# Kernel tuning notes

Measured on AMD Instinct MI355X. Metric: run time of the kernel, lower is better.

Reference implementation:

```python
import jax, jax.numpy as jnp
import numpy as np

N_NODES = 50000
N_EDGES = 800000
IN_DIM = 128
ADD = 8
HIDDEN = 256
OUT_DIM = 128


def gcn_conv(x, src, dst, W, b, n_nodes):
    """PyG GCNConv: linear -> sym-normalized scatter-add with self-loops -> bias."""
    loop = jnp.arange(n_nodes, dtype=src.dtype)
    s = jnp.concatenate([src, loop])
    d = jnp.concatenate([dst, loop])
    deg = jax.ops.segment_sum(jnp.ones(s.shape[0], dtype=x.dtype), d, num_segments=n_nodes)
    dinv = jnp.where(deg > 0, jax.lax.rsqrt(deg), 0.0)
    norm = dinv[s] * dinv[d]                       # [E+N]
    h = x @ W                                      # [N, F_out]
    msg = h[s] * norm[:, None]                     # [E+N, F_out]
    out = jax.ops.segment_sum(msg, d, num_segments=n_nodes)
    return out + b


def prelu(x, a):
    return jnp.where(x >= 0, x, a * x)


def setup_inputs() -> dict:
    key = jax.random.key(0)
    ks = jax.random.split(key, 8)
    x = jax.random.normal(ks[0], (N_NODES, IN_DIM), dtype=jnp.float32)
    edge_index = jax.random.randint(ks[1], (2, N_EDGES), 0, N_NODES, dtype=jnp.int64)
    id_vec = jax.random.normal(ks[2], (ADD,), dtype=jnp.float32)
    # Glorot-ish init for linear weights, PReLU slope 0.25 (torch default)
    W1 = jax.random.normal(ks[3], (IN_DIM + ADD, HIDDEN), dtype=jnp.float32) * 0.05
    b1 = jnp.zeros((HIDDEN,), dtype=jnp.float32)
    a1 = jnp.full((HIDDEN,), 0.25, dtype=jnp.float32)
    W2 = jax.random.normal(ks[4], (HIDDEN, OUT_DIM), dtype=jnp.float32) * 0.05
    b2 = jnp.zeros((OUT_DIM,), dtype=jnp.float32)
    a2 = jnp.full((OUT_DIM,), 0.25, dtype=jnp.float32)
    return {"x": x, "edge_index": edge_index, "id": id_vec,
            "W1": W1, "b1": b1, "a1": a1, "W2": W2, "b2": b2, "a2": a2}


def reference(x, edge_index, id, W1, b1, a1, W2, b2, a2):
    n = x.shape[0]
    src, dst = edge_index[0], edge_index[1]
    # tile id vector onto every node and concat along features
    xi = jnp.concatenate([x, jnp.broadcast_to(id[None, :], (n, id.shape[0]))], axis=1)
    h = gcn_conv(xi, src, dst, W1, b1, n)
    h = prelu(h, a1)
    h = gcn_conv(h, src, dst, W2, b2, n)
    h = prelu(h, a2)
    return h
```

## Files before the change

### kernel.cpp

```cpp
#include <hip/hip_runtime.h>


constexpr int NN = 50000;
constexpr int NE = 800000;
constexpr int NBUCK = 196;
constexpr int TILE = 2048;
constexpr int NSCAT = (NE + TILE - 1) / TILE;
constexpr int NAGG = NN / 4;

typedef __attribute__((ext_vector_type(8))) short short8;
typedef __attribute__((ext_vector_type(4))) float floatx4;

__device__ inline void bsplit(float v, unsigned short& hi, unsigned short& lo) {
  unsigned u = __float_as_uint(v);
  hi = (unsigned short)(u >> 16);
  float rem = v - __uint_as_float(u & 0xffff0000u);
  lo = (unsigned short)(__float_as_uint(rem) >> 16);
}

__device__ inline unsigned short bf16_rtne(float v) {
  unsigned u = __float_as_uint(v);
  return (unsigned short)((u + 0x7fffu + ((u >> 16) & 1u)) >> 16);
}

__device__ inline float bflo(unsigned u) { return __uint_as_float(u << 16); }
__device__ inline float bfhi(unsigned u) { return __uint_as_float(u & 0xffff0000u); }

template <int K, int N>
__device__ inline void pack_one(const float* __restrict__ W, unsigned short* __restrict__ Bhi,
                                unsigned short* __restrict__ Blo, int id) {
  constexpr int KC = K / 32;
  int j = id & 7;
  int lane = (id >> 3) & 63;
  int rest = id >> 9;
  int c = rest % KC;
  int nt = rest / KC;
  int k = c * 32 + (lane >> 4) * 8 + j;
  int n = nt * 16 + (lane & 15);
  unsigned short hi, lo;
  bsplit(W[(size_t)k * N + n], hi, lo);
  Bhi[id] = hi;
  Blo[id] = lo;
}

__global__ __launch_bounds__(256) void front_kernel(
    const int* __restrict__ ei, int* __restrict__ tilecnt,
    const float* __restrict__ W1, const float* __restrict__ W2,
    const float* __restrict__ idv,
    unsigned short* __restrict__ B1hi, unsigned short* __restrict__ B1lo,
    unsigned short* __restrict__ B2hi, unsigned short* __restrict__ B2lo,
    float* __restrict__ cvec) {
  int t = threadIdx.x;
  if (blockIdx.x < NSCAT) {
    __shared__ int h[NBUCK];
    for (int i = t; i < NBUCK; i += 256) h[i] = 0;
    __syncthreads();
    int base = blockIdx.x * TILE;
    int end = base + TILE; if (end > NE) end = NE;
    for (int e = base + t; e < end; e += 256) atomicAdd(&h[ei[NE + e] >> 8], 1);
    __syncthreads();
    for (int i = t; i < NBUCK; i += 256) tilecnt[blockIdx.x * NBUCK + i] = h[i];
  } else {
    int id = (blockIdx.x - NSCAT) * 256 + t;
    if (id < 32768) {
      pack_one<128, 256>(W1, B1hi, B1lo, id);
    } else if (id < 65536) {
      pack_one<256, 128>(W2, B2hi, B2lo, id - 32768);
    } else if (id < 65536 + 256) {
      int m = id - 65536;
      float c = 0.f;
#pragma unroll
      for (int j = 0; j < 8; ++j) c += idv[j] * W1[(128 + j) * 256 + m];
      cvec[m] = c;
    }
  }
}

__global__ __launch_bounds__(256) void tile_scan_a_kernel(const int* __restrict__ tilecnt,
                                                          int* __restrict__ tpre,
                                                          int* __restrict__ bcnt) {
  __shared__ int sm[256];
  int b = blockIdx.x, t = threadIdx.x;
  int i0 = 2 * t, i1 = 2 * t + 1;
  int v0 = (i0 < NSCAT) ? tilecnt[i0 * NBUCK + b] : 0;
  int v1 = (i1 < NSCAT) ? tilecnt[i1 * NBUCK + b] : 0;
  int s = v0 + v1;
  sm[t] = s;
  __syncthreads();
  for (int off = 1; off < 256; off <<= 1) {
    int u = (t >= off) ? sm[t - off] : 0;
    __syncthreads();
    sm[t] += u;
    __syncthreads();
  }
  int ex = sm[t] - s;
  if (i0 < NSCAT) tpre[i0 * NBUCK + b] = ex;
  if (i1 < NSCAT) tpre[i1 * NBUCK + b] = ex + v0;
  if (t == 255) bcnt[b] = sm[255];
}

__global__ __launch_bounds__(256) void bucket_scatter_kernel(
    const int* __restrict__ ei, const int* __restrict__ tilecnt,
    const int* __restrict__ tpre, const int* __restrict__ bcnt,
    unsigned* __restrict__ ebuf) {
  __shared__ int lbase[NBUCK], gb[NBUCK], lcur[NBUCK], ssc[256], bscan[256];
  __shared__ unsigned stage[TILE];
  int t = threadIdx.x;
  int tile = blockIdx.x;
  int base = tile * TILE;
  int cntTile = NE - base; if (cntTile > TILE) cntTile = TILE;
  int bv = (t < NBUCK) ? bcnt[t] : 0;
  bscan[t] = bv;
  int h = (t < NBUCK) ? tilecnt[tile * NBUCK + t] : 0;
  ssc[t] = h;
  __syncthreads();
  for (int off = 1; off < 256; off <<= 1) {
    int u1 = (t >= off) ? ssc[t - off] : 0;
    int u2 = (t >= off) ? bscan[t - off] : 0;
    __syncthreads();
    ssc[t] += u1;
    bscan[t] += u2;
    __syncthreads();
  }
  if (t < NBUCK) {
    int ex = ssc[t] - h;
    lbase[t] = ex;
    lcur[t] = ex;
    gb[t] = (bscan[t] - bv) + tpre[tile * NBUCK + t];
  }
  __syncthreads();
  for (int e = base + t; e < base + cntTile; e += 256) {
    int s = ei[e];
    int d = ei[NE + e];
    int b = d >> 8;
    int pos = atomicAdd(&lcur[b], 1);
    stage[pos] = ((unsigned)(d & 255) << 16) | (unsigned)s;
  }
  __syncthreads();
  for (int i = t; i < cntTile; i += 256) {
    int lo = 0, hi = NBUCK - 1;
    while (lo < hi) {
      int mid = (lo + hi + 1) >> 1;
      if (lbase[mid] <= i) lo = mid; else hi = mid - 1;
    }
    ebuf[gb[lo] + (i - lbase[lo])] = stage[i];
  }
}

__global__ __launch_bounds__(256) void bucket_csr_kernel(
    const unsigned* __restrict__ ebuf, const int* __restrict__ bcnt,
    const float* __restrict__ x,
    int* __restrict__ offs, int* __restrict__ col,
    float* __restrict__ dinv, unsigned short* __restrict__ xsb) {
  __shared__ int cnt[256], cur[256], sums[256], bscan[256];
  __shared__ float dinvs[256];
  __shared__ int g0s;
  int b = blockIdx.x, t = threadIdx.x;
  int node0 = b << 8;
  cnt[t] = 0;
  int bv = (t < NBUCK) ? bcnt[t] : 0;
  bscan[t] = bv;
  __syncthreads();
  for (int off = 1; off < 256; off <<= 1) {
    int u = (t >= off) ? bscan[t - off] : 0;
    __syncthreads();
    bscan[t] += u;
    __syncthreads();
  }
  if (t == b) g0s = bscan[t] - bv;
  __syncthreads();
  int g0 = g0s, g1 = g0 + bcnt[b];
  for (int i = g0 + t; i < g1; i += 256) atomicAdd(&cnt[ebuf[i] >> 16], 1);
  __syncthreads();
  int c = cnt[t];
  sums[t] = c;
  __syncthreads();
  for (int off = 1; off < 256; off <<= 1) {
    int u = (t >= off) ? sums[t - off] : 0;
    __syncthreads();
    sums[t] += u;
    __syncthreads();
  }
  int ex = sums[t] - c;
  cur[t] = ex;
  float dval = rsqrtf((float)(c + 1));
  dinvs[t] = dval;
  int node = node0 + t;
  if (node < NN) {
    offs[node] = g0 + ex;
    dinv[node] = dval;
  }
  __syncthreads();
  for (int i = g0 + t; i < g1; i += 256) {
    unsigned v = ebuf[i];
    int pos = atomicAdd(&cur[v >> 16], 1);
    col[g0 + pos] = (int)(v & 0xffffu);
  }
  for (int i = t; i < 256 * 32; i += 256) {
    int ln = i >> 5;
    int n2 = node0 + ln;
    if (n2 >= NN) continue;
    float dd = dinvs[ln];
    float4 v = ((const float4*)x)[(size_t)n2 * 32 + (i & 31)];
    ushort4 o;
    o.x = bf16_rtne(v.x * dd);
    o.y = bf16_rtne(v.y * dd);
    o.z = bf16_rtne(v.z * dd);
    o.w = bf16_rtne(v.w * dd);
    ((ushort4*)xsb)[(size_t)n2 * 32 + (i & 31)] = o;
  }
  if (b == 0 && t == 0) offs[NN] = NE;
}

template <int MODE>
__global__ __launch_bounds__(256) void agg_kernel(
    const unsigned short* __restrict__ in, const float* __restrict__ dinv,
    const int* __restrict__ offs, const int* __restrict__ col,
    const float* __restrict__ bias, const float* __restrict__ alpha,
    unsigned short* __restrict__ outhi, unsigned short* __restrict__ outlo,
    float* __restrict__ outf, float* __restrict__ Svec) {
  int t = threadIdx.x;
  if (MODE == 0 && blockIdx.x >= NAGG) {
    int d = (blockIdx.x - NAGG) * 256 + t;
    if (d < NN) {
      float s = 0.f;
      int end = offs[d + 1];
      for (int p = offs[d]; p < end; ++p) s += dinv[col[p]];
      float dd = dinv[d];
      Svec[d] = dd * (dd + s);
    }
    return;
  }
  const uint2* inb = (const uint2*)in;
  int node = blockIdx.x * 4 + (t >> 6);
  int lane = t & 63;
  int r = lane & 31;
  int half = lane >> 5;
  int beg = offs[node], end = offs[node + 1];

  float4 a0 = make_float4(0.f, 0.f, 0.f, 0.f);
  float4 a1 = make_float4(0.f, 0.f, 0.f, 0.f);
  float4 a2 = make_float4(0.f, 0.f, 0.f, 0.f);
  float4 a3 = make_float4(0.f, 0.f, 0.f, 0.f);
  int p = beg + half;
  for (; p + 14 < end; p += 16) {
    int s0 = col[p];      int s1 = col[p + 2];
    int s2 = col[p + 4];  int s3 = col[p + 6];
    int s4 = col[p + 8];  int s5 = col[p + 10];
    int s6 = col[p + 12]; int s7 = col[p + 14];
    uint2 v0 = inb[(size_t)s0 * 32 + r];
    uint2 v1 = inb[(size_t)s1 * 32 + r];
    uint2 v2 = inb[(size_t)s2 * 32 + r];
    uint2 v3 = inb[(size_t)s3 * 32 + r];
    uint2 v4 = inb[(size_t)s4 * 32 + r];
    uint2 v5 = inb[(size_t)s5 * 32 + r];
    uint2 v6 = inb[(size_t)s6 * 32 + r];
    uint2 v7 = inb[(size_t)s7 * 32 + r];
    a0.x += bflo(v0.x); a0.y += bfhi(v0.x); a0.z += bflo(v0.y); a0.w += bfhi(v0.y);
    a1.x += bflo(v1.x); a1.y += bfhi(v1.x); a1.z += bflo(v1.y); a1.w += bfhi(v1.y);
    a2.x += bflo(v2.x); a2.y += bfhi(v2.x); a2.z += bflo(v2.y); a2.w += bfhi(v2.y);
    a3.x += bflo(v3.x); a3.y += bfhi(v3.x); a3.z += bflo(v3.y); a3.w += bfhi(v3.y);
    a0.x += bflo(v4.x); a0.y += bfhi(v4.x); a0.z += bflo(v4.y); a0.w += bfhi(v4.y);
    a1.x += bflo(v5.x); a1.y += bfhi(v5.x); a1.z += bflo(v5.y); a1.w += bfhi(v5.y);
    a2.x += bflo(v6.x); a2.y += bfhi(v6.x); a2.z += bflo(v6.y); a2.w += bfhi(v6.y);
    a3.x += bflo(v7.x); a3.y += bfhi(v7.x); a3.z += bflo(v7.y); a3.w += bfhi(v7.y);
  }
  for (; p + 2 < end; p += 4) {
    int s0 = col[p];
    int s1 = col[p + 2];
    uint2 v0 = inb[(size_t)s0 * 32 + r];
    uint2 v1 = inb[(size_t)s1 * 32 + r];
    a0.x += bflo(v0.x); a0.y += bfhi(v0.x); a0.z += bflo(v0.y); a0.w += bfhi(v0.y);
    a1.x += bflo(v1.x); a1.y += bfhi(v1.x); a1.z += bflo(v1.y); a1.w += bfhi(v1.y);
  }
  if (p < end) {
    uint2 v0 = inb[(size_t)col[p] * 32 + r];
    a0.x += bflo(v0.x); a0.y += bfhi(v0.x); a0.z += bflo(v0.y); a0.w += bfhi(v0.y);
  }
  float4 acc = make_float4((a0.x + a1.x) + (a2.x + a3.x), (a0.y + a1.y) + (a2.y + a3.y),
                           (a0.z + a1.z) + (a2.z + a3.z), (a0.w + a1.w) + (a2.w + a3.w));
  acc.x += __shfl_xor(acc.x, 32);
  acc.y += __shfl_xor(acc.y, 32);
  acc.z += __shfl_xor(acc.z, 32);
  acc.w += __shfl_xor(acc.w, 32);

  float dd = dinv[node];
  if (half == 0) {
    uint2 sv = inb[(size_t)node * 32 + r];
    acc.x = dd * (acc.x + bflo(sv.x));
    acc.y = dd * (acc.y + bfhi(sv.x));
    acc.z = dd * (acc.z + bflo(sv.y));
    acc.w = dd * (acc.w + bfhi(sv.y));
    if (MODE == 0) {
      ushort4 h4, l4;
      bsplit(acc.x, h4.x, l4.x);
      bsplit(acc.y, h4.y, l4.y);
      bsplit(acc.z, h4.z, l4.z);
      bsplit(acc.w, h4.w, l4.w);
      ((ushort4*)outhi)[(size_t)node * 32 + r] = h4;
      ((ushort4*)outlo)[(size_t)node * 32 + r] = l4;
    } else {
      float4 b = ((const float4*)bias)[r];
      float4 al = ((const float4*)alpha)[r];
      acc.x += b.x; acc.y += b.y; acc.z += b.z; acc.w += b.w;
      acc.x = (acc.x >= 0.f) ? acc.x : al.x * acc.x;
      acc.y = (acc.y >= 0.f) ? acc.y : al.y * acc.y;
      acc.z = (acc.z >= 0.f) ? acc.z : al.z * acc.z;
      acc.w = (acc.w >= 0.f) ? acc.w : al.w * acc.w;
      ((float4*)outf)[(size_t)node * 32 + r] = acc;
    }
  }
}

template <int K, int N, int MODE, int ASPLIT>
__global__ __launch_bounds__(256) void gemm_mfma_kernel(
    const unsigned short* __restrict__ Ahi, const unsigned short* __restrict__ Alo,
    const unsigned short* __restrict__ Bhi, const unsigned short* __restrict__ Blo,
    const float* __restrict__ Svec, const float* __restrict__ cvec,
    const float* __restrict__ bias, const float* __restrict__ alpha,
    const float* __restrict__ rowscale, unsigned short* __restrict__ Cb) {
  constexpr int KC = K / 32;
  constexpr int NT = N / 16;
  int wave = threadIdx.x >> 6;
  int lane = threadIdx.x & 63;
  int row0 = blockIdx.x * 64 + wave * 16;
  if (row0 >= NN) return;
  int m = lane & 15, quad = lane >> 4;
  int arow = row0 + m;

  short8 ah[KC], al[KC];
  const unsigned short* ap = Ahi + (size_t)arow * K + quad * 8;
#pragma unroll
  for (int c = 0; c < KC; ++c) ah[c] = *(const short8*)(ap + c * 32);
  if (ASPLIT) {
    const unsigned short* alp = Alo + (size_t)arow * K + quad * 8;
#pragma unroll
    for (int c = 0; c < KC; ++c) al[c] = *(const short8*)(alp + c * 32);
  }

  float sv[4];
#pragma unroll
  for (int i = 0; i < 4; ++i) {
    int r = row0 + quad * 4 + i;
    sv[i] = (MODE == 1) ? Svec[r] : rowscale[r];
  }

#pragma unroll 1
  for (int nt = 0; nt < NT; ++nt) {
    floatx4 acc = {0.f, 0.f, 0.f, 0.f};
#pragma unroll
    for (int c = 0; c < KC; ++c) {
      short8 bh = *(const short8*)(Bhi + ((size_t)(nt * KC + c) * 64 + lane) * 8);
      short8 bl = *(const short8*)(Blo + ((size_t)(nt * KC + c) * 64 + lane) * 8);
      acc = __builtin_amdgcn_mfma_f32_16x16x32_bf16(ah[c], bh, acc, 0, 0, 0);
      acc = __builtin_amdgcn_mfma_f32_16x16x32_bf16(ah[c], bl, acc, 0, 0, 0);
      if (ASPLIT) acc = __builtin_amdgcn_mfma_f32_16x16x32_bf16(al[c], bh, acc, 0, 0, 0);
    }
    int c0 = nt * 16 + m;
    if (MODE == 1) {
      float cv = cvec[c0], bb = bias[c0], aa = alpha[c0];
#pragma unroll
      for (int i = 0; i < 4; ++i) {
        int r = row0 + quad * 4 + i;
        float v = acc[i] + sv[i] * cv + bb;
        v = (v >= 0.f) ? v : aa * v;
        Cb[(size_t)r * N + c0] = bf16_rtne(v);
      }
    } else {
#pragma unroll
      for (int i = 0; i < 4; ++i) {
        int r = row0 + quad * 4 + i;
        Cb[(size_t)r * N + c0] = bf16_rtne(acc[i] * sv[i]);
      }
    }
  }
}

extern "C" void kernel_launch(void* const* d_in, const int* in_sizes, int n_in,
                              void* d_out, int out_size, void* d_ws, size_t ws_size,
                              hipStream_t stream) {
  const float* x = (const float*)d_in[0];
  const int* ei = (const int*)d_in[1];
  const float* idv = (const float*)d_in[2];
  const float* W1 = (const float*)d_in[3];
  const float* b1 = (const float*)d_in[4];
  const float* a1 = (const float*)d_in[5];
  const float* W2 = (const float*)d_in[6];
  const float* b2 = (const float*)d_in[7];
  const float* a2 = (const float*)d_in[8];
  float* out = (float*)d_out;

  char* w = (char*)d_ws;
  size_t off = 0;
  auto alloc = [&](size_t bytes) -> void* {
    void* p = w + off;
    off += bytes;
    off = (off + 255) & ~(size_t)255;
    return p;
  };
  int* tilecnt = (int*)alloc((size_t)NSCAT * NBUCK * 4);
  int* tpre = (int*)alloc((size_t)NSCAT * NBUCK * 4);
  int* bcnt = (int*)alloc((size_t)NBUCK * 4);
  unsigned* ebuf = (unsigned*)alloc((size_t)NE * 4);
  float* dinv = (float*)alloc((size_t)NN * 4);
  float* Svec = (float*)alloc((size_t)NN * 4);
  int* offs = (int*)alloc((size_t)(NN + 1) * 4);
  int* col = (int*)alloc((size_t)NE * 4);
  float* cvec = (float*)alloc(256 * 4);
  unsigned short* xsb = (unsigned short*)alloc((size_t)NN * 128 * 2);
  unsigned short* aggxhi = (unsigned short*)alloc((size_t)NN * 128 * 2);
  unsigned short* aggxlo = (unsigned short*)alloc((size_t)NN * 128 * 2);
  unsigned short* h1b = (unsigned short*)alloc((size_t)NN * 256 * 2);
  unsigned short* h2b = (unsigned short*)alloc((size_t)NN * 128 * 2);
  unsigned short* B1hi = (unsigned short*)alloc(128 * 256 * 2);
  unsigned short* B1lo = (unsigned short*)alloc(128 * 256 * 2);
  unsigned short* B2hi = (unsigned short*)alloc(256 * 128 * 2);
  unsigned short* B2lo = (unsigned short*)alloc(256 * 128 * 2);

  front_kernel<<<NSCAT + 257, 256, 0, stream>>>(ei, tilecnt, W1, W2, idv,
                                                B1hi, B1lo, B2hi, B2lo, cvec);
  tile_scan_a_kernel<<<NBUCK, 256, 0, stream>>>(tilecnt, tpre, bcnt);
  bucket_scatter_kernel<<<NSCAT, 256, 0, stream>>>(ei, tilecnt, tpre, bcnt, ebuf);
  bucket_csr_kernel<<<NBUCK, 256, 0, stream>>>(ebuf, bcnt, x, offs, col, dinv, xsb);
  agg_kernel<0><<<NAGG + NBUCK, 256, 0, stream>>>(xsb, dinv, offs, col, nullptr, nullptr,
                                                  aggxhi, aggxlo, nullptr, Svec);
  gemm_mfma_kernel<128, 256, 1, 1><<<(NN + 63) / 64, 256, 0, stream>>>(
      aggxhi, aggxlo, B1hi, B1lo, Svec, cvec, b1, a1, nullptr, h1b);
  gemm_mfma_kernel<256, 128, 2, 0><<<(NN + 63) / 64, 256, 0, stream>>>(
      h1b, nullptr, B2hi, B2lo, nullptr, nullptr, nullptr, nullptr, dinv, h2b);
  agg_kernel<1><<<NAGG, 256, 0, stream>>>(h2b, dinv, offs, col, b2, a2,
                                          nullptr, nullptr, out, nullptr);
}
```

Before: 276.3 us.

## Fuse layer-1 aggregation with first GEMM via shared-memory staging

The first-layer neighbor aggregation and the first MFMA GEMM are merged into one kernel. Each 512-thread block aggregates 32 nodes into an LDS tile, splits the values into hi/lo bf16 in registers, and runs the 3-pass MFMA product directly. This removes the aggxhi/aggxlo intermediate round trip through global memory and one launch. The Svec computation moves into its own small kernel, which adds a launch and lowers per-block parallelism during the gather phase.

Result: no change. 280.9 us (+1.6%).

```diff
diff --git a/kernel.cpp b/kernel.cpp
--- a/kernel.cpp
+++ b/kernel.cpp
@@ -6,7 +6,6 @@
 constexpr int NBUCK = 196;
 constexpr int TILE = 2048;
 constexpr int NSCAT = (NE + TILE - 1) / TILE;
-constexpr int NAGG = NN / 4;
 
 typedef __attribute__((ext_vector_type(8))) short short8;
 typedef __attribute__((ext_vector_type(4))) float floatx4;
@@ -212,26 +211,195 @@
   if (b == 0 && t == 0) offs[NN] = NE;
 }
 
-template <int MODE>
-__global__ __launch_bounds__(256) void agg_kernel(
+__global__ void svec_kernel(const float* __restrict__ dinv, const int* __restrict__ offs,
+                            const int* __restrict__ col, float* __restrict__ Svec) {
+  int d = blockIdx.x * blockDim.x + threadIdx.x;
+  if (d >= NN) return;
+  float s = 0.f;
+  int end = offs[d + 1];
+  for (int p = offs[d]; p < end; ++p) s += dinv[col[p]];
+  float dd = dinv[d];
+  Svec[d] = dd * (dd + s);
+}
+
+__global__ __launch_bounds__(512, 8) void aggmm1_kernel(
+    const unsigned short* __restrict__ xsb, const float* __restrict__ dinv,
+    const int* __restrict__ offs, const int* __restrict__ col,
+    const unsigned short* __restrict__ B1hi, const unsigned short* __restrict__ B1lo,
+    const float* __restrict__ Svec, const float* __restrict__ cvec,
+    const float* __restrict__ bias, const float* __restrict__ alpha,
+    unsigned short* __restrict__ h1b) {
+  __shared__ float As[32][132];
+  const uint2* inb = (const uint2*)xsb;
+  int t = threadIdx.x;
+  int w = t >> 6;
+  int lane = t & 63;
+  int r = lane & 31;
+  int half = lane >> 5;
+
+  for (int round = 0; round < 4; ++round) {
+    int ln = round * 8 + w;
+    int node = blockIdx.x * 32 + ln;
+    if (node < NN) {
+      int beg = offs[node], end = offs[node + 1];
+      float4 a0 = make_float4(0.f, 0.f, 0.f, 0.f);
+      float4 a1 = make_float4(0.f, 0.f, 0.f, 0.f);
+      float4 a2 = make_float4(0.f, 0.f, 0.f, 0.f);
+      float4 a3 = make_float4(0.f, 0.f, 0.f, 0.f);
+      int p = beg + half;
+      for (; p + 14 < end; p += 16) {
+        int s0 = col[p];      int s1 = col[p + 2];
+        int s2 = col[p + 4];  int s3 = col[p + 6];
+        int s4 = col[p + 8];  int s5 = col[p + 10];
+        int s6 = col[p + 12]; int s7 = col[p + 14];
+        uint2 v0 = inb[(size_t)s0 * 32 + r];
+        uint2 v1 = inb[(size_t)s1 * 32 + r];
+        uint2 v2 = inb[(size_t)s2 * 32 + r];
+        uint2 v3 = inb[(size_t)s3 * 32 + r];
+        uint2 v4 = inb[(size_t)s4 * 32 + r];
+        uint2 v5 = inb[(size_t)s5 * 32 + r];
+        uint2 v6 = inb[(size_t)s6 * 32 + r];
+        uint2 v7 = inb[(size_t)s7 * 32 + r];
+        a0.x += bflo(v0.x); a0.y += bfhi(v0.x); a0.z += bflo(v0.y); a0.w += bfhi(v0.y);
+        a1.x += bflo(v1.x); a1.y += bfhi(v1.x); a1.z += bflo(v1.y); a1.w += bfhi(v1.y);
+        a2.x += bflo(v2.x); a2.y += bfhi(v2.x); a2.z += bflo(v2.y); a2.w += bfhi(v2.y);
+        a3.x += bflo(v3.x); a3.y += bfhi(v3.x); a3.z += bflo(v3.y); a3.w += bfhi(v3.y);
+        a0.x += bflo(v4.x); a0.y += bfhi(v4.x); a0.z += bflo(v4.y); a0.w += bfhi(v4.y);
+        a1.x += bflo(v5.x); a1.y += bfhi(v5.x); a1.z += bflo(v5.y); a1.w += bfhi(v5.y);
+        a2.x += bflo(v6.x); a2.y += bfhi(v6.x); a2.z += bflo(v6.y); a2.w += bfhi(v6.y);
+        a3.x += bflo(v7.x); a3.y += bfhi(v7.x); a3.z += bflo(v7.y); a3.w += bfhi(v7.y);
+      }
+      for (; p + 2 < end; p += 4) {
+        int s0 = col[p];
+        int s1 = col[p + 2];
+        uint2 v0 = inb[(size_t)s0 * 32 + r];
+        uint2 v1 = inb[(size_t)s1 * 32 + r];
+        a0.x += bflo(v0.x); a0.y += bfhi(v0.x); a0.z += bflo(v0.y); a0.w += bfhi(v0.y);
+        a1.x += bflo(v1.x); a1.y += bfhi(v1.x); a1.z += bflo(v1.y); a1.w += bfhi(v1.y);
+      }
+      if (p < end) {
+        uint2 v0 = inb[(size_t)col[p] * 32 + r];
+        a0.x += bflo(v0.x); a0.y += bfhi(v0.x); a0.z += bflo(v0.y); a0.w += bfhi(v0.y);
+      }
+      float4 acc = make_float4((a0.x + a1.x) + (a2.x + a3.x), (a0.y + a1.y) + (a2.y + a3.y),
+                               (a0.z + a1.z) + (a2.z + a3.z), (a0.w + a1.w) + (a2.w + a3.w));
+      acc.x += __shfl_xor(acc.x, 32);
+      acc.y += __shfl_xor(acc.y, 32);
+      acc.z += __shfl_xor(acc.z, 32);
+      acc.w += __shfl_xor(acc.w, 32);
+      float dd = dinv[node];
+      if (half == 0) {
+        uint2 sv2 = inb[(size_t)node * 32 + r];
+        acc.x = dd * (acc.x + bflo(sv2.x));
+        acc.y = dd * (acc.y + bfhi(sv2.x));
+        acc.z = dd * (acc.z + bflo(sv2.y));
+        acc.w = dd * (acc.w + bfhi(sv2.y));
+        *(float4*)&As[ln][r * 4] = acc;
+      }
+    }
+  }
+  __syncthreads();
+
+  int m = lane & 15, quad = lane >> 4;
+  int g = w & 1;
+  int q4 = w >> 1;
+  int row0 = blockIdx.x * 32 + g * 16;
+  int arow = g * 16 + m;
+
+  short8 ah[4], al[4];
+#pragma unroll
+  for (int c = 0; c < 4; ++c) {
+    const float* ap = &As[arow][c * 32 + quad * 8];
+    float4 f0 = *(const float4*)ap;
+    float4 f1 = *(const float4*)(ap + 4);
+    float ff[8] = {f0.x, f0.y, f0.z, f0.w, f1.x, f1.y, f1.z, f1.w};
+#pragma unroll
+    for (int j = 0; j < 8; ++j) {
+      unsigned u = __float_as_uint(ff[j]);
+      ah[c][j] = (short)(u >> 16);
+      float rem = ff[j] - __uint_as_float(u & 0xffff0000u);
+      al[c][j] = (short)(__float_as_uint(rem) >> 16);
+    }
+  }
+  float sv[4];
+#pragma unroll
+  for (int i = 0; i < 4; ++i) {
+    int rr = row0 + quad * 4 + i;
+    sv[i] = Svec[rr < NN ? rr : (NN - 1)];
+  }
+#pragma unroll
+  for (int ntl = 0; ntl < 4; ++ntl) {
+    int nt = q4 * 4 + ntl;
+    floatx4 acc = {0.f, 0.f, 0.f, 0.f};
+#pragma unroll
+    for (int c = 0; c < 4; ++c) {
+      short8 bh = *(const short8*)(B1hi + ((size_t)(nt * 4 + c) * 64 + lane) * 8);
+      short8 bl = *(const short8*)(B1lo + ((size_t)(nt * 4 + c) * 64 + lane) * 8);
+      acc = __builtin_amdgcn_mfma_f32_16x16x32_bf16(ah[c], bh, acc, 0, 0, 0);
+      acc = __builtin_amdgcn_mfma_f32_16x16x32_bf16(ah[c], bl, acc, 0, 0, 0);
+      acc = __builtin_amdgcn_mfma_f32_16x16x32_bf16(al[c], bh, acc, 0, 0, 0);
+    }
+    int c0 = nt * 16 + m;
+    float cv = cvec[c0], bb = bias[c0], aa = alpha[c0];
+#pragma unroll
+    for (int i = 0; i < 4; ++i) {
+      int rr = row0 + quad * 4 + i;
+      if (rr < NN) {
+        float v = acc[i] + sv[i] * cv + bb;
+        v = (v >= 0.f) ? v : aa * v;
+        h1b[(size_t)rr * 256 + c0] = bf16_rtne(v);
+      }
+    }
+  }
+}
+
+__global__ __launch_bounds__(256) void gemm2_kernel(
+    const unsigned short* __restrict__ Ab,
+    const unsigned short* __restrict__ Bhi, const unsigned short* __restrict__ Blo,
+    const float* __restrict__ rowscale, unsigned short* __restrict__ Cb) {
+  constexpr int K = 256, N = 128, KC = K / 32, NT = N / 16;
+  int wave = threadIdx.x >> 6;
+  int lane = threadIdx.x & 63;
+  int row0 = blockIdx.x * 64 + wave * 16;
+  if (row0 >= NN) return;
+  int m = lane & 15, quad = lane >> 4;
+  int arow = row0 + m;
+
+  short8 ah[KC];
+  const unsigned short* ap = Ab + (size_t)arow * K + quad * 8;
+#pragma unroll
+  for (int c = 0; c < KC; ++c) ah[c] = *(const short8*)(ap + c * 32);
+
+  float sv[4];
+#pragma unroll
+  for (int i = 0; i < 4; ++i) sv[i] = rowscale[row0 + quad * 4 + i];
+
+#pragma unroll 1
+  for (int nt = 0; nt < NT; ++nt) {
+    floatx4 acc = {0.f, 0.f, 0.f, 0.f};
+#pragma unroll
+    for (int c = 0; c < KC; ++c) {
+      short8 bh = *(const short8*)(Bhi + ((size_t)(nt * KC + c) * 64 + lane) * 8);
+      short8 bl = *(const short8*)(Blo + ((size_t)(nt * KC + c) * 64 + lane) * 8);
+      acc = __builtin_amdgcn_mfma_f32_16x16x32_bf16(ah[c], bh, acc, 0, 0, 0);
+      acc = __builtin_amdgcn_mfma_f32_16x16x32_bf16(ah[c], bl, acc, 0, 0, 0);
+    }
+    int c0 = nt * 16 + m;
+#pragma unroll
+    for (int i = 0; i < 4; ++i) {
+      int r = row0 + quad * 4 + i;
+      Cb[(size_t)r * N + c0] = bf16_rtne(acc[i] * sv[i]);
+    }
+  }
+}
+
+__global__ __launch_bounds__(256) void agg2_kernel(
     const unsigned short* __restrict__ in, const float* __restrict__ dinv,
     const int* __restrict__ offs, const int* __restrict__ col,
     const float* __restrict__ bias, const float* __restrict__ alpha,
-    unsigned short* __restrict__ outhi, unsigned short* __restrict__ outlo,
-    float* __restrict__ outf, float* __restrict__ Svec) {
+    float* __restrict__ outf) {
+  const uint2* inb = (const uint2*)in;
   int t = threadIdx.x;
-  if (MODE == 0 && blockIdx.x >= NAGG) {
-    int d = (blockIdx.x - NAGG) * 256 + t;
-    if (d < NN) {
-      float s = 0.f;
-      int end = offs[d + 1];
-      for (int p = offs[d]; p < end; ++p) s += dinv[col[p]];
-      float dd = dinv[d];
-      Svec[d] = dd * (dd + s);
-    }
-    return;
-  }
-  const uint2* inb = (const uint2*)in;
   int node = blockIdx.x * 4 + (t >> 6);
   int lane = t & 63;
   int r = lane & 31;
@@ -286,93 +454,19 @@
 
   float dd = dinv[node];
   if (half == 0) {
-    uint2 sv = inb[(size_t)node * 32 + r];
-    acc.x = dd * (acc.x + bflo(sv.x));
-    acc.y = dd * (acc.y + bfhi(sv.x));
-    acc.z = dd * (acc.z + bflo(sv.y));
-    acc.w = dd * (acc.w + bfhi(sv.y));
-    if (MODE == 0) {
-      ushort4 h4, l4;
-      bsplit(acc.x, h4.x, l4.x);
-      bsplit(acc.y, h4.y, l4.y);
-      bsplit(acc.z, h4.z, l4.z);
-      bsplit(acc.w, h4.w, l4.w);
-      ((ushort4*)outhi)[(size_t)node * 32 + r] = h4;
-      ((ushort4*)outlo)[(size_t)node * 32 + r] = l4;
-    } else {
-      float4 b = ((const float4*)bias)[r];
-      float4 al = ((const float4*)alpha)[r];
-      acc.x += b.x; acc.y += b.y; acc.z += b.z; acc.w += b.w;
-      acc.x = (acc.x >= 0.f) ? acc.x : al.x * acc.x;
-      acc.y = (acc.y >= 0.f) ? acc.y : al.y * acc.y;
-      acc.z = (acc.z >= 0.f) ? acc.z : al.z * acc.z;
-      acc.w = (acc.w >= 0.f) ? acc.w : al.w * acc.w;
-      ((float4*)outf)[(size_t)node * 32 + r] = acc;
-    }
-  }
-}
-
-template <int K, int N, int MODE, int ASPLIT>
-__global__ __launch_bounds__(256) void gemm_mfma_kernel(
-    const unsigned short* __restrict__ Ahi, const unsigned short* __restrict__ Alo,
-    const unsigned short* __restrict__ Bhi, const unsigned short* __restrict__ Blo,
-    const float* __restrict__ Svec, const float* __restrict__ cvec,
-    const float* __restrict__ bias, const float* __restrict__ alpha,
-    const float* __restrict__ rowscale, unsigned short* __restrict__ Cb) {
-  constexpr int KC = K / 32;
-  constexpr int NT = N / 16;
-  int wave = threadIdx.x >> 6;
-  int lane = threadIdx.x & 63;
-  int row0 = blockIdx.x * 64 + wave * 16;
-  if (row0 >= NN) return;
-  int m = lane & 15, quad = lane >> 4;
-  int arow = row0 + m;
-
-  short8 ah[KC], al[KC];
-  const unsigned short* ap = Ahi + (size_t)arow * K + quad * 8;
-#pragma unroll
-  for (int c = 0; c < KC; ++c) ah[c] = *(const short8*)(ap + c * 32);
-  if (ASPLIT) {
-    const unsigned short* alp = Alo + (size_t)arow * K + quad * 8;
-#pragma unroll
-    for (int c = 0; c < KC; ++c) al[c] = *(const short8*)(alp + c * 32);
-  }
-
-  float sv[4];
-#pragma unroll
-  for (int i = 0; i < 4; ++i) {
-    int r = row0 + quad * 4 + i;
-    sv[i] = (MODE == 1) ? Svec[r] : rowscale[r];
-  }
-
-#pragma unroll 1
-  for (int nt = 0; nt < NT; ++nt) {
-    floatx4 acc = {0.f, 0.f, 0.f, 0.f};
-#pragma unroll
-    for (int c = 0; c < KC; ++c) {
-      short8 bh = *(const short8*)(Bhi + ((size_t)(nt * KC + c) * 64 + lane) * 8);
-      short8 bl = *(const short8*)(Blo + ((size_t)(nt * KC + c) * 64 + lane) * 8);
-      acc = __builtin_amdgcn_mfma_f32_16x16x32_bf16(ah[c], bh, acc, 0, 0, 0);
-      acc = __builtin_amdgcn_mfma_f32_16x16x32_bf16(ah[c], bl, acc, 0, 0, 0);
-      if (ASPLIT) acc = __builtin_amdgcn_mfma_f32_16x16x32_bf16(al[c], bh, acc, 0, 0, 0);
-    }
-    int c0 = nt * 16 + m;
-    if (MODE == 1) {
-      float cv = cvec[c0], bb = bias[c0], aa = alpha[c0];
-#pragma unroll
-      for (int i = 0; i < 4; ++i) {
-        int r = row0 + quad * 4 + i;
-        float v = acc[i] + sv[i] * cv + bb;
-        v = (v >= 0.f) ? v : aa * v;
-        Cb[(size_t)r * N + c0] = bf16_rtne(v);
-      }
-    } else {
-#pragma unroll
-      for (int i = 0; i < 4; ++i) {
-        int r = row0 + quad * 4 + i;
-        Cb[(size_t)r * N + c0] = bf16_rtne(acc[i] * sv[i]);
-      }
-    }
+    uint2 sv2 = inb[(size_t)node * 32 + r];
+    acc.x = dd * (acc.x + bflo(sv2.x));
+    acc.y = dd * (acc.y + bfhi(sv2.x));
+    acc.z = dd * (acc.z + bflo(sv2.y));
+    acc.w = dd * (acc.w + bfhi(sv2.y));
+    float4 b = ((const float4*)bias)[r];
+    float4 al = ((const float4*)alpha)[r];
+    acc.x += b.x; acc.y += b.y; acc.z += b.z; acc.w += b.w;
+    acc.x = (acc.x >= 0.f) ? acc.x : al.x * acc.x;
+    acc.y = (acc.y >= 0.f) ? acc.y : al.y * acc.y;
+    acc.z = (acc.z >= 0.f) ? acc.z : al.z * acc.z;
+    acc.w = (acc.w >= 0.f) ? acc.w : al.w * acc.w;
+    ((float4*)outf)[(size_t)node * 32 + r] = acc;
   }
 }
 
@@ -408,8 +502,6 @@
   int* col = (int*)alloc((size_t)NE * 4);
   float* cvec = (float*)alloc(256 * 4);
   unsigned short* xsb = (unsigned short*)alloc((size_t)NN * 128 * 2);
-  unsigned short* aggxhi = (unsigned short*)alloc((size_t)NN * 128 * 2);
-  unsigned short* aggxlo = (unsigned short*)alloc((size_t)NN * 128 * 2);
   unsigned short* h1b = (unsigned short*)alloc((size_t)NN * 256 * 2);
   unsigned short* h2b = (unsigned short*)alloc((size_t)NN * 128 * 2);
   unsigned short* B1hi = (unsigned short*)alloc(128 * 256 * 2);
@@ -422,12 +514,9 @@
   tile_scan_a_kernel<<<NBUCK, 256, 0, stream>>>(tilecnt, tpre, bcnt);
   bucket_scatter_kernel<<<NSCAT, 256, 0, stream>>>(ei, tilecnt, tpre, bcnt, ebuf);
   bucket_csr_kernel<<<NBUCK, 256, 0, stream>>>(ebuf, bcnt, x, offs, col, dinv, xsb);
-  agg_kernel<0><<<NAGG + NBUCK, 256, 0, stream>>>(xsb, dinv, offs, col, nullptr, nullptr,
-                                                  aggxhi, aggxlo, nullptr, Svec);
-  gemm_mfma_kernel<128, 256, 1, 1><<<(NN + 63) / 64, 256, 0, stream>>>(
-      aggxhi, aggxlo, B1hi, B1lo, Svec, cvec, b1, a1, nullptr, h1b);
-  gemm_mfma_kernel<256, 128, 2, 0><<<(NN + 63) / 64, 256, 0, stream>>>(
-      h1b, nullptr, B2hi, B2lo, nullptr, nullptr, nullptr, nullptr, dinv, h2b);
-  agg_kernel<1><<<NAGG, 256, 0, stream>>>(h2b, dinv, offs, col, b2, a2,
-                                          nullptr, nullptr, out, nullptr);
-}
+  svec_kernel<<<(NN + 255) / 256, 256, 0, stream>>>(dinv, offs, col, Svec);
+  aggmm1_kernel<<<(NN + 31) / 32, 512, 0, stream>>>(xsb, dinv, offs, col,
+                                                    B1hi, B1lo, Svec, cvec, b1, a1, h1b);
+  gemm2_kernel<<<(NN + 63) / 64, 256, 0, stream>>>(h1b, B2hi, B2lo, dinv, h2b);
+  agg2_kernel<<<NN / 4, 256, 0, stream>>>(h2b, dinv, offs, col, b2, a2, out);
+}
```
